# Kernel optimization log

Hardware: AMD Instinct MI355X
Metric: run time of the kernel (lower is better)

Reference implementation:

```python
import jax, jax.numpy as jnp
import numpy as np
import math

B, T, C = 64, 1024, 12
D, H, L = 512, 8, 2
FFN = 4 * D
FC_HIDDEN, NUM_CLASSES = 256, 5
KERNEL = 25          # config.moving_average default
FACTOR = 3           # config.autocorrelation_factor default
TOP_K = int(FACTOR * math.log(T))
EPS = 1e-5
MIN_SCALE = 1e-10


def _sinusoidal_pos(n_pos, dim):
    # HF AutoformerSinusoidalPositionalEmbedding._init_weight (Marian-style: sin block then cos block)
    pos = np.arange(n_pos, dtype=np.float64)[:, None]
    j = np.arange(dim)[None, :]
    enc = pos / np.power(10000.0, 2 * (j // 2) / dim)
    half = dim // 2
    out = np.zeros((n_pos, dim), np.float32)
    out[:, :half] = np.sin(enc[:, 0::2])
    out[:, half:] = np.cos(enc[:, 1::2])
    return jnp.asarray(out)


def _layernorm(x, g, b):
    mu = jnp.mean(x, axis=-1, keepdims=True)
    var = jnp.mean(jnp.square(x - mu), axis=-1, keepdims=True)
    return (x - mu) * jax.lax.rsqrt(var + EPS) * g + b


def _series_decomp_seasonal(x):
    # moving-average trend with edge-replication padding; return seasonal = x - trend
    pad = (KERNEL - 1) // 2
    xp = jnp.pad(x, ((0, 0), (pad, pad), (0, 0)), mode='edge')
    cs = jnp.cumsum(xp, axis=1)
    cs = jnp.concatenate([jnp.zeros_like(cs[:, :1]), cs], axis=1)
    trend = (cs[:, KERNEL:] - cs[:, :-KERNEL]) / KERNEL
    return x - trend


def _autocorr_attention(h, w, b):
    # w: (4, D, D) q/k/v/out, b: (4, D). Eval-mode HF AutoformerAttention (per-batch delays).
    hd = D // H
    def split(t):
        return t.reshape(B, T, H, hd).transpose(0, 2, 1, 3)  # (B,H,T,hd)
    q = split(h @ w[0] + b[0])
    k = split(h @ w[1] + b[1])
    v = split(h @ w[2] + b[2])
    # period-based dependency discovery via FFT cross-correlation along time
    qf = jnp.fft.rfft(q, n=T, axis=2)
    kf = jnp.fft.rfft(k, n=T, axis=2)
    corr = jnp.fft.irfft(qf * jnp.conj(kf), n=T, axis=2)  # (B,H,T,hd)
    mean_corr = corr.mean(axis=(1, 3))                    # (B,T)
    top_vals, top_idx = jax.lax.top_k(mean_corr, TOP_K)   # (B,K)
    wts = jax.nn.softmax(top_vals, axis=-1)               # (B,K)
    t_idx = jnp.arange(T)
    agg = jnp.zeros_like(v)
    for i in range(TOP_K):  # small fixed K, mirrors HF loop; circular roll by -delay
        idx = (t_idx[None, :] + top_idx[:, i][:, None]) % T      # (B,T)
        rolled = jnp.take_along_axis(v, idx[:, None, :, None], axis=2)
        agg = agg + rolled * wts[:, i][:, None, None, None]
    out = agg.transpose(0, 2, 1, 3).reshape(B, T, D)
    return out @ w[3] + b[3]


def _forward(x, emb_w, emb_ln_g, emb_ln_b, attn_w, attn_b, ln_g, ln_b,
             fc1_w, fc1_b, fc2_w, fc2_b, head_w1, head_b1, head_w2, head_b2):
    # AutoformerMeanScaler (observed mask is all-ones): scale = mean |x| over time, loc = 0
    scale = jnp.clip(jnp.mean(jnp.abs(x), axis=1, keepdims=True), MIN_SCALE)  # (B,1,C)
    inputs = x / scale
    # static features: log1p(|loc|)=0 and log(scale), broadcast over time; lags=[0] -> lagged == inputs
    static = jnp.concatenate([jnp.zeros_like(scale), jnp.log(scale)], axis=-1)  # (B,1,2C)
    feats = jnp.broadcast_to(static, (B, T, 2 * C))
    ti = jnp.concatenate([inputs, feats], axis=-1)  # (B,T,3C)

    h = ti @ emb_w + _sinusoidal_pos(T, D)[None]
    h = _layernorm(h, emb_ln_g, emb_ln_b)

    for l in range(L):
        res = h
        a = _autocorr_attention(h, attn_w[l], attn_b[l])
        h = _layernorm(res + a, ln_g[l, 0], ln_b[l, 0])
        h = _series_decomp_seasonal(h)
        res = h
        f = jax.nn.gelu(h @ fc1_w[l] + fc1_b[l], approximate=False)
        h = res + f @ fc2_w[l] + fc2_b[l]
        h = _layernorm(h, ln_g[l, 1], ln_b[l, 1])
        h = _series_decomp_seasonal(h)

    feat = h.mean(axis=1)  # (B,D)
    return jax.nn.relu(feat @ head_w1 + head_b1) @ head_w2 + head_b2  # (B,num_classes)


def setup_inputs() -> dict:
    key = jax.random.key(0)
    ks = jax.random.split(key, 8)
    s = 0.02
    rn = lambda k, shape: jax.random.normal(k, shape, jnp.float32) * s
    return {
        'x': jax.random.normal(ks[0], (B, T, C), jnp.float32),
        'emb_w': rn(ks[1], (3 * C, D)),
        'emb_ln_g': jnp.ones((D,), jnp.float32),
        'emb_ln_b': jnp.zeros((D,), jnp.float32),
        'attn_w': rn(ks[2], (L, 4, D, D)),
        'attn_b': jnp.zeros((L, 4, D), jnp.float32),
        'ln_g': jnp.ones((L, 2, D), jnp.float32),
        'ln_b': jnp.zeros((L, 2, D), jnp.float32),
        'fc1_w': rn(ks[3], (L, D, FFN)),
        'fc1_b': jnp.zeros((L, FFN), jnp.float32),
        'fc2_w': rn(ks[4], (L, FFN, D)),
        'fc2_b': jnp.zeros((L, D), jnp.float32),
        'head_w1': rn(ks[5], (D, FC_HIDDEN)),
        'head_b1': jnp.zeros((FC_HIDDEN,), jnp.float32),
        'head_w2': rn(ks[6], (FC_HIDDEN, NUM_CLASSES)),
        'head_b2': jnp.zeros((NUM_CLASSES,), jnp.float32),
    }


def reference(x, emb_w, emb_ln_g, emb_ln_b, attn_w, attn_b, ln_g, ln_b,
              fc1_w, fc1_b, fc2_w, fc2_b, head_w1, head_b1, head_w2, head_b2):
    return _forward(x, emb_w, emb_ln_g, emb_ln_b, attn_w, attn_b, ln_g, ln_b,
                    fc1_w, fc1_b, fc2_w, fc2_b, head_w1, head_b1, head_w2, head_b2)
```

## Files before the change

### kernel.cpp

```cpp
#include <hip/hip_runtime.h>
#include <math.h>

#define CB 64
#define CT 1024
#define CCH 12
#define CD 512
#define CL 2
#define CFFN 2048
#define CFCH 256
#define CNC 5
#define CTOPK 20
#define CEPS 1e-5f

typedef __attribute__((ext_vector_type(8))) short bfrag;
typedef __attribute__((ext_vector_type(4))) float ffrag;

__device__ inline ushort bf16r(float f) {
  unsigned u = __float_as_uint(f);
  unsigned r = (u + 0x7FFFu + ((u >> 16) & 1u)) >> 16;
  return (ushort)r;
}
__device__ inline float bf16f(ushort h) { return __uint_as_float(((unsigned)h) << 16); }

__device__ __forceinline__ void gld16(const ushort* g, ushort* l) {
  __builtin_amdgcn_global_load_lds((__attribute__((address_space(1))) void*)g,
                                   (__attribute__((address_space(3))) void*)l,
                                   16, 0, 0);
}

struct c32 { float x, y; };
__device__ inline c32 cadd(c32 a, c32 b) { return c32{a.x + b.x, a.y + b.y}; }
__device__ inline c32 csub(c32 a, c32 b) { return c32{a.x - b.x, a.y - b.y}; }
__device__ inline c32 cmul(c32 a, c32 b) {
  return c32{a.x * b.x - a.y * b.y, a.x * b.y + a.y * b.x};
}
__device__ inline c32 cmulj(c32 a, c32 b) {
  return c32{a.x * b.x + a.y * b.y, a.y * b.x - a.x * b.y};
}
__device__ inline c32 mineg_i(c32 a) { return c32{a.y, -a.x}; }
__device__ inline c32 mul_i(c32 a) { return c32{-a.y, a.x}; }

#define ZIDX(p) ((p) + ((p) >> 4))

__device__ inline int drev4(int t) {
  return ((t & 3) << 8) | (((t >> 2) & 3) << 6) | (((t >> 4) & 3) << 4) |
         (((t >> 6) & 3) << 2) | ((t >> 8) & 3);
}

template <int INV>
__device__ inline void fft_stage(c32* zz, const c32* twl, int tid, int s) {
  int L = 1 << (2 * s);
  int j = tid & (L - 1);
  int g = tid >> (2 * s);
  int p0 = (g << (2 * s + 2)) + j;
  int tb = j << (8 - 2 * s);
  c32 w1 = twl[ZIDX(tb)], w2 = twl[ZIDX(2 * tb)], w3 = twl[ZIDX(3 * tb)];
  c32 b0 = zz[ZIDX(p0)], b1 = zz[ZIDX(p0 + L)], b2 = zz[ZIDX(p0 + 2 * L)],
      b3 = zz[ZIDX(p0 + 3 * L)];
  if (INV) { b1 = cmulj(b1, w1); b2 = cmulj(b2, w2); b3 = cmulj(b3, w3); }
  else     { b1 = cmul(b1, w1);  b2 = cmul(b2, w2);  b3 = cmul(b3, w3); }
  c32 e0 = cadd(b0, b2), e1 = csub(b0, b2), e2 = cadd(b1, b3), e3 = csub(b1, b3);
  c32 e3r = INV ? mul_i(e3) : mineg_i(e3);
  zz[ZIDX(p0)] = cadd(e0, e2);
  zz[ZIDX(p0 + L)] = cadd(e1, e3r);
  zz[ZIDX(p0 + 2 * L)] = csub(e0, e2);
  zz[ZIDX(p0 + 3 * L)] = csub(e1, e3r);
}

__device__ inline void unp_acc(const c32* zf, int w, c32& acc) {
  int wc = (1024 - w) & 1023;
  c32 Z1 = zf[ZIDX(w)];
  c32 Z2r = zf[ZIDX(wc)];
  c32 Z2 = c32{Z2r.x, -Z2r.y};
  c32 Qf = c32{0.5f * (Z1.x + Z2.x), 0.5f * (Z1.y + Z2.y)};
  c32 M = c32{Z1.x - Z2.x, Z1.y - Z2.y};
  c32 Kf = c32{0.5f * M.y, -0.5f * M.x};
  acc.x += Qf.x * Kf.x + Qf.y * Kf.y;
  acc.y += Qf.y * Kf.x - Qf.x * Kf.y;
}

__global__ __launch_bounds__(256) void k_twid(c32* __restrict__ tw) {
  int j = blockIdx.x * 256 + threadIdx.x;
  double a = -2.0 * 3.14159265358979323846 * (double)j / 1024.0;
  tw[j] = c32{(float)cos(a), (float)sin(a)};
}

__global__ __launch_bounds__(256) void k_scale(const float* __restrict__ x,
                                               float* __restrict__ sc,
                                               float* __restrict__ lg) {
  int b = blockIdx.x, tid = threadIdx.x;
  float acc[CCH];
#pragma unroll
  for (int c = 0; c < CCH; ++c) acc[c] = 0.f;
  const float* xb = x + (size_t)b * CT * CCH;
  for (int t = tid; t < CT; t += 256) {
    const float* row = xb + t * CCH;
#pragma unroll
    for (int c = 0; c < CCH; ++c) acc[c] += fabsf(row[c]);
  }
  __shared__ float red[256][CCH];
#pragma unroll
  for (int c = 0; c < CCH; ++c) red[tid][c] = acc[c];
  __syncthreads();
  for (int off = 128; off > 0; off >>= 1) {
    if (tid < off) {
#pragma unroll
      for (int c = 0; c < CCH; ++c) red[tid][c] += red[tid + off][c];
    }
    __syncthreads();
  }
  if (tid < CCH) {
    float s = fmaxf(red[0][tid] * (1.0f / CT), 1e-10f);
    sc[b * CCH + tid] = s;
    lg[b * CCH + tid] = logf(s);
  }
}

__global__ __launch_bounds__(512) void k_postab(float* __restrict__ pos) {
  int t = blockIdx.x;
  int d = threadIdx.x;
  double v;
  if (d < 256) {
    double w = pow(10000.0, -((double)d) / 256.0);
    v = sin((double)t * w);
  } else {
    double w = pow(10000.0, -((double)(d - 256)) / 256.0);
    v = cos((double)t * w);
  }
  pos[(size_t)t * CD + d] = (float)v;
}

__global__ __launch_bounds__(128) void k_embed(const float* __restrict__ x,
                                               const float* __restrict__ sc,
                                               const float* __restrict__ lg,
                                               const float* __restrict__ W,
                                               const float* __restrict__ postab,
                                               const float* __restrict__ g,
                                               const float* __restrict__ beta,
                                               float* __restrict__ h,
                                               ushort* __restrict__ h2) {
  int row = blockIdx.x;
  int b = row >> 10, t = row & 1023;
  int tid = threadIdx.x;
  __shared__ float xs[CCH], ls[CCH];
  if (tid < CCH) {
    float s = sc[b * CCH + tid];
    xs[tid] = x[(size_t)row * CCH + tid] / s;
    ls[tid] = lg[b * CCH + tid];
  }
  __syncthreads();
  int d0 = tid * 4;
  float4 p = *(const float4*)(postab + (size_t)t * CD + d0);
  float v0 = p.x, v1 = p.y, v2 = p.z, v3 = p.w;
#pragma unroll
  for (int c = 0; c < CCH; ++c) {
    float xc = xs[c], lc = ls[c];
    float4 w0 = *(const float4*)(W + (size_t)c * CD + d0);
    float4 w1 = *(const float4*)(W + (size_t)(24 + c) * CD + d0);
    v0 += xc * w0.x + lc * w1.x;
    v1 += xc * w0.y + lc * w1.y;
    v2 += xc * w0.z + lc * w1.z;
    v3 += xc * w0.w + lc * w1.w;
  }
  float s1 = v0 + v1 + v2 + v3;
  float s2 = v0 * v0 + v1 * v1 + v2 * v2 + v3 * v3;
  for (int off = 32; off > 0; off >>= 1) {
    s1 += __shfl_down(s1, off);
    s2 += __shfl_down(s2, off);
  }
  __shared__ float ws1[2], ws2[2], mv[2];
  int wid = tid >> 6, lane = tid & 63;
  if (lane == 0) { ws1[wid] = s1; ws2[wid] = s2; }
  __syncthreads();
  if (tid == 0) {
    float S1 = ws1[0] + ws1[1], S2 = ws2[0] + ws2[1];
    float mu = S1 * (1.0f / CD);
    float var = S2 * (1.0f / CD) - mu * mu;
    mv[0] = mu;
    mv[1] = 1.0f / sqrtf(var + CEPS);
  }
  __syncthreads();
  float mu = mv[0], ri = mv[1];
  float4 gg = *(const float4*)(g + d0);
  float4 bb = *(const float4*)(beta + d0);
  float4 o;
  o.x = (v0 - mu) * ri * gg.x + bb.x;
  o.y = (v1 - mu) * ri * gg.y + bb.y;
  o.z = (v2 - mu) * ri * gg.z + bb.z;
  o.w = (v3 - mu) * ri * gg.w + bb.w;
  *(float4*)(h + (size_t)row * CD + d0) = o;
  ushort4 hv = {bf16r(o.x), bf16r(o.y), bf16r(o.z), bf16r(o.w)};
  *(ushort4*)(h2 + (size_t)row * CD + d0) = hv;
}

__global__ __launch_bounds__(256) void k_cvtw(const float* __restrict__ W,
                                              ushort* __restrict__ W2,
                                              int K, int N) {
  __shared__ float tile[32][33];
  int tx = threadIdx.x & 31, ty = threadIdx.x >> 5;
  int n0 = blockIdx.x * 32, k0 = blockIdx.y * 32;
#pragma unroll
  for (int r = 0; r < 4; ++r)
    tile[ty * 4 + r][tx] = W[(size_t)(k0 + ty * 4 + r) * N + n0 + tx];
  __syncthreads();
#pragma unroll
  for (int r = 0; r < 4; ++r) {
    int nl = ty * 4 + r, kl = tx;
    W2[(size_t)(n0 + nl) * K + k0 + kl] = bf16r(tile[kl][nl]);
  }
}

template <int EPI>
__global__ __launch_bounds__(256) void k_gemm3(const ushort* __restrict__ A,
                                               const ushort* __restrict__ W,
                                               const float* __restrict__ bias,
                                               const float* __restrict__ R,
                                               float* __restrict__ Cf,
                                               ushort* __restrict__ Cs,
                                               ushort* __restrict__ Cs2,
                                               int lda, int ldb, int ldc, int K) {
  __shared__ ushort AhS[2][128 * 32];
  __shared__ ushort BhS[2][128 * 32];
  int tid = threadIdx.x;
  int n0 = blockIdx.x * 128, m0 = blockIdx.y * 128;
  int wid = __builtin_amdgcn_readfirstlane(tid >> 6);
  int lane = tid & 63;
  int lr = lane >> 2;
  int lc = ((lane & 3) ^ ((lr >> 2) & 3)) * 8;
  int wm = wid >> 1, wn = wid & 1;
  int mOff = wm * 64, nOff = wn * 64;
  int quad = lane >> 4, l16 = lane & 15;

  const ushort* pA = A + (size_t)(m0 + wid * 32 + lr) * lda + lc;
  const ushort* pB = W + (size_t)(n0 + wid * 32 + lr) * ldb + lc;
  const int NK = K >> 5;

  ffrag acc[4][4];
#pragma unroll
  for (int i = 0; i < 4; ++i)
#pragma unroll
    for (int j = 0; j < 4; ++j) acc[i][j] = (ffrag)(0.f);

#define ISSUE(t, buf)                                                        \
  {                                                                          \
    int kk = (t) << 5;                                                       \
    ushort* lA = &AhS[buf][(wid * 32) * 32];                                 \
    ushort* lB = &BhS[buf][(wid * 32) * 32];                                 \
    gld16(pA + kk, lA);                                                      \
    gld16(pA + (size_t)16 * lda + kk, lA + 16 * 32);                         \
    gld16(pB + kk, lB);                                                      \
    gld16(pB + (size_t)16 * ldb + kk, lB + 16 * 32);                         \
  }

  ISSUE(0, 0);
  ISSUE(1, 1);
  for (int k = 0; k < NK; ++k) {
    if (k + 1 < NK) {
      asm volatile("s_waitcnt vmcnt(4)\n\ts_barrier" ::: "memory");
    } else {
      asm volatile("s_waitcnt vmcnt(0)\n\ts_barrier" ::: "memory");
    }
    int buf = k & 1;
    bfrag ah[4], bh[4];
#pragma unroll
    for (int i = 0; i < 4; ++i) {
      int row = mOff + i * 16 + l16;
      ah[i] = *(const bfrag*)&AhS[buf][row * 32 + (quad ^ ((row >> 2) & 3)) * 8];
    }
#pragma unroll
    for (int j = 0; j < 4; ++j) {
      int row = nOff + j * 16 + l16;
      bh[j] = *(const bfrag*)&BhS[buf][row * 32 + (quad ^ ((row >> 2) & 3)) * 8];
    }
#pragma unroll
    for (int i = 0; i < 4; ++i)
#pragma unroll
      for (int j = 0; j < 4; ++j)
        acc[i][j] = __builtin_amdgcn_mfma_f32_16x16x32_bf16(ah[i], bh[j], acc[i][j], 0, 0, 0);
    asm volatile("s_barrier" ::: "memory");
    if (k + 2 < NK) ISSUE(k + 2, buf);
  }
#undef ISSUE

#pragma unroll
  for (int j = 0; j < 4; ++j) {
    int col = n0 + nOff + j * 16 + l16;
    float bcol = bias[col];
#pragma unroll
    for (int i = 0; i < 4; ++i) {
      int rowb = m0 + mOff + i * 16 + quad * 4;
      if (EPI == 7) {
        if (col < 1024) {
          float4 o = {acc[i][j][0] + bcol, acc[i][j][1] + bcol,
                      acc[i][j][2] + bcol, acc[i][j][3] + bcol};
          *(float4*)(Cf + (size_t)col * ldc + rowb) = o;
        } else {
          float* Vf = (float*)Cs;
#pragma unroll
          for (int r = 0; r < 4; ++r)
            Vf[(size_t)(rowb + r) * 512 + (col - 1024)] = acc[i][j][r] + bcol;
        }
      } else {
#pragma unroll
        for (int r = 0; r < 4; ++r) {
          int row = rowb + r;
          float vv = acc[i][j][r] + bcol;
          if (EPI == 1) vv = 0.5f * vv * (1.0f + erff(vv * 0.7071067811865475f));
          if (EPI == 2) vv += R[(size_t)row * ldc + col];
          if (EPI == 1) {
            Cs[(size_t)row * ldc + col] = bf16r(vv);
          } else {
            Cf[(size_t)row * ldc + col] = vv;
          }
        }
      }
    }
  }
}

__global__ __launch_bounds__(256) void k_fft(const float* __restrict__ QT,
                                             const c32* __restrict__ twg,
                                             c32* __restrict__ part, int Mc) {
  __shared__ c32 z[4][1088];
  __shared__ c32 twl[1088];
  int dg = blockIdx.x, zb = blockIdx.y, tid = threadIdx.x;
#pragma unroll
  for (int k = 0; k < 4; ++k) {
    int i = tid + k * 256;
    twl[ZIDX(i)] = twg[i];
  }
  c32 pa = {0.f, 0.f}, pb = {0.f, 0.f}, p5 = {0.f, 0.f};
  for (int i = 0; i < 4; ++i) {
    int d0 = dg * 16 + i * 4;
#pragma unroll
    for (int f = 0; f < 4; ++f) {
      const float* qr = QT + (size_t)(d0 + f) * Mc + (size_t)zb * 1024;
      const float* kr = QT + (size_t)(512 + d0 + f) * Mc + (size_t)zb * 1024;
#pragma unroll
      for (int k = 0; k < 4; ++k) {
        int t = tid + k * 256;
        z[f][ZIDX(drev4(t))] = c32{qr[t], kr[t]};
      }
    }
    __syncthreads();
    for (int s = 0; s < 5; ++s) {
#pragma unroll
      for (int f = 0; f < 4; ++f) fft_stage<0>(&z[f][0], twl, tid, s);
      __syncthreads();
    }
#pragma unroll
    for (int f = 0; f < 4; ++f) {
      unp_acc(&z[f][0], tid, pa);
      unp_acc(&z[f][0], tid + 256, pb);
      if (tid == 0) unp_acc(&z[f][0], 512, p5);
    }
    __syncthreads();
  }
  c32* po = part + ((size_t)zb * 32 + dg) * 513;
  po[tid] = pa;
  po[tid + 256] = pb;
  if (tid == 0) po[512] = p5;
}

__global__ __launch_bounds__(256) void k_spectopk(const c32* __restrict__ part,
                                                  const c32* __restrict__ twg,
                                                  float* __restrict__ wts,
                                                  int* __restrict__ idxs) {
  int b = blockIdx.x, tid = threadIdx.x;
  __shared__ c32 twl[1088];
  __shared__ c32 S[1024];
  __shared__ c32 zz[1088];
  __shared__ float corr[1024];
#pragma unroll
  for (int k = 0; k < 4; ++k) {
    int i = tid + k * 256;
    twl[ZIDX(i)] = twg[i];
  }
  c32 sa = {0.f, 0.f}, sb = {0.f, 0.f}, s5 = {0.f, 0.f};
  const c32* pbase = part + (size_t)b * 32 * 513;
  for (int p = 0; p < 32; ++p) {
    const c32* pp = pbase + p * 513;
    sa = cadd(sa, pp[tid]);
    sb = cadd(sb, pp[tid + 256]);
    if (tid == 0) s5 = cadd(s5, pp[512]);
  }
  S[tid] = sa;
  S[tid + 256] = sb;
  if (tid == 0) S[512] = s5;
  if (tid > 0) S[1024 - tid] = c32{sa.x, -sa.y};
  S[768 - tid] = c32{sb.x, -sb.y};
  __syncthreads();
#pragma unroll
  for (int k = 0; k < 4; ++k) {
    int t = tid + k * 256;
    zz[ZIDX(drev4(t))] = S[t];
  }
  __syncthreads();
  for (int s = 0; s < 5; ++s) {
    fft_stage<1>(&zz[0], twl, tid, s);
    __syncthreads();
  }
  const float scl = 1.0f / (1024.0f * 512.0f);
#pragma unroll
  for (int k = 0; k < 4; ++k) {
    int t = tid + k * 256;
    corr[t] = zz[ZIDX(t)].x * scl;
  }
  __syncthreads();
  __shared__ float swv[4];
  __shared__ int swi[4];
  __shared__ float selv[CTOPK];
  __shared__ int seli[CTOPK];
  int wid = tid >> 6, lane = tid & 63;
  for (int k = 0; k < CTOPK; ++k) {
    float bv = -INFINITY;
    int bi = 0;
#pragma unroll
    for (int q = 0; q < 4; ++q) {
      int idx = tid + q * 256;
      float v = corr[idx];
      if (v > bv || (v == bv && idx < bi)) { bv = v; bi = idx; }
    }
#pragma unroll
    for (int off = 32; off > 0; off >>= 1) {
      float ov = __shfl_down(bv, off);
      int oi = __shfl_down(bi, off);
      if (ov > bv || (ov == bv && oi < bi)) { bv = ov; bi = oi; }
    }
    if (lane == 0) { swv[wid] = bv; swi[wid] = bi; }
    __syncthreads();
    if (tid == 0) {
      float mvv = swv[0];
      int mi = swi[0];
      for (int q2 = 1; q2 < 4; ++q2)
        if (swv[q2] > mvv || (swv[q2] == mvv && swi[q2] < mi)) { mvv = swv[q2]; mi = swi[q2]; }
      selv[k] = mvv;
      seli[k] = mi;
      corr[mi] = -INFINITY;
    }
    __syncthreads();
  }
  if (tid == 0) {
    float mx = selv[0], sum = 0.f, e[CTOPK];
    for (int k = 0; k < CTOPK; ++k) {
      e[k] = expf(selv[k] - mx);
      sum += e[k];
    }
    float inv = 1.0f / sum;
    for (int k = 0; k < CTOPK; ++k) {
      wts[b * CTOPK + k] = e[k] * inv;
      idxs[b * CTOPK + k] = seli[k];
    }
  }
}

__global__ __launch_bounds__(128) void k_agg(const float* __restrict__ Vf,
                                             const float* __restrict__ wts,
                                             const int* __restrict__ idxs,
                                             ushort* __restrict__ out2) {
  int nb = gridDim.x;
  int blk = blockIdx.x;
  int row = (blk & 7) * (nb >> 3) + (blk >> 3);
  int b = row >> 10, t = row & 1023;
  int d0 = threadIdx.x * 4;
  const float* Vb = Vf + (size_t)b * CT * 512;
  float4 acc = {0.f, 0.f, 0.f, 0.f};
#pragma unroll
  for (int k = 0; k < CTOPK; ++k) {
    float w = wts[b * CTOPK + k];
    int r = t + idxs[b * CTOPK + k];
    if (r >= CT) r -= CT;
    float4 v = *(const float4*)(Vb + (size_t)r * 512 + d0);
    acc.x += w * v.x;
    acc.y += w * v.y;
    acc.z += w * v.z;
    acc.w += w * v.w;
  }
  ushort4 hv = {bf16r(acc.x), bf16r(acc.y), bf16r(acc.z), bf16r(acc.w)};
  *(ushort4*)(out2 + (size_t)row * CD + d0) = hv;
}

template <int ADD>
__global__ __launch_bounds__(128) void k_ln(const float* __restrict__ X,
                                            const float* __restrict__ Rr,
                                            const float* __restrict__ g,
                                            const float* __restrict__ beta,
                                            float* __restrict__ out) {
  int row = blockIdx.x, tid = threadIdx.x;
  int d0 = tid * 4;
  float4 v = *(const float4*)(X + (size_t)row * CD + d0);
  if (ADD) {
    float4 r = *(const float4*)(Rr + (size_t)row * CD + d0);
    v.x += r.x; v.y += r.y; v.z += r.z; v.w += r.w;
  }
  float s1 = v.x + v.y + v.z + v.w;
  float s2 = v.x * v.x + v.y * v.y + v.z * v.z + v.w * v.w;
  for (int off = 32; off > 0; off >>= 1) {
    s1 += __shfl_down(s1, off);
    s2 += __shfl_down(s2, off);
  }
  __shared__ float ws1[2], ws2[2], mv[2];
  int wid = tid >> 6, lane = tid & 63;
  if (lane == 0) { ws1[wid] = s1; ws2[wid] = s2; }
  __syncthreads();
  if (tid == 0) {
    float S1 = ws1[0] + ws1[1], S2 = ws2[0] + ws2[1];
    float mu = S1 * (1.0f / CD);
    float var = S2 * (1.0f / CD) - mu * mu;
    mv[0] = mu;
    mv[1] = 1.0f / sqrtf(var + CEPS);
  }
  __syncthreads();
  float mu = mv[0], ri = mv[1];
  float4 gg = *(const float4*)(g + d0);
  float4 bb = *(const float4*)(beta + d0);
  float4 o;
  o.x = (v.x - mu) * ri * gg.x + bb.x;
  o.y = (v.y - mu) * ri * gg.y + bb.y;
  o.z = (v.z - mu) * ri * gg.z + bb.z;
  o.w = (v.w - mu) * ri * gg.w + bb.w;
  *(float4*)(out + (size_t)row * CD + d0) = o;
}

__global__ __launch_bounds__(128) void k_decomp(const float* __restrict__ X,
                                                float* __restrict__ out,
                                                ushort* __restrict__ out2) {
  int nb = gridDim.x;
  int blk = blockIdx.x;
  int row = (blk & 7) * (nb >> 3) + (blk >> 3);
  int b = row >> 10, t = row & 1023;
  int d0 = threadIdx.x * 4;
  const float* xb = X + (size_t)b * CT * CD + d0;
  float4 s = {0.f, 0.f, 0.f, 0.f};
#pragma unroll
  for (int j = -12; j <= 12; ++j) {
    int tt = t + j;
    tt = tt < 0 ? 0 : (tt > CT - 1 ? CT - 1 : tt);
    float4 v = *(const float4*)(xb + (size_t)tt * CD);
    s.x += v.x; s.y += v.y; s.z += v.z; s.w += v.w;
  }
  float4 xv = *(const float4*)(xb + (size_t)t * CD);
  const float inv = 1.0f / 25.0f;
  float4 o = {xv.x - s.x * inv, xv.y - s.y * inv, xv.z - s.z * inv, xv.w - s.w * inv};
  *(float4*)(out + (size_t)row * CD + d0) = o;
  ushort4 hv = {bf16r(o.x), bf16r(o.y), bf16r(o.z), bf16r(o.w)};
  *(ushort4*)(out2 + (size_t)row * CD + d0) = hv;
}

__global__ __launch_bounds__(256) void k_meanp(const float* __restrict__ X,
                                               float* __restrict__ part) {
  int b = blockIdx.x, g = blockIdx.y, tid = threadIdx.x;
  const float* xb = X + (size_t)b * CT * CD + (size_t)g * 128 * CD;
  float a0 = 0.f, a1 = 0.f;
  for (int r = 0; r < 128; ++r) {
    a0 += xb[(size_t)r * CD + tid];
    a1 += xb[(size_t)r * CD + tid + 256];
  }
  part[((size_t)b * 8 + g) * CD + tid] = a0;
  part[((size_t)b * 8 + g) * CD + tid + 256] = a1;
}

__global__ __launch_bounds__(256) void k_headf(const float* __restrict__ part,
                                               const float* __restrict__ w1,
                                               const float* __restrict__ b1,
                                               const float* __restrict__ w2,
                                               const float* __restrict__ b2,
                                               float* __restrict__ out) {
  int b = blockIdx.x, tid = threadIdx.x;
  __shared__ float f[CD];
  __shared__ float hid[CFCH];
  for (int d = tid; d < CD; d += 256) {
    float s = 0.f;
#pragma unroll
    for (int g = 0; g < 8; ++g) s += part[((size_t)b * 8 + g) * CD + d];
    f[d] = s * (1.0f / CT);
  }
  __syncthreads();
  float a = b1[tid];
  for (int d = 0; d < CD; ++d) a += f[d] * w1[d * CFCH + tid];
  hid[tid] = fmaxf(a, 0.f);
  __syncthreads();
  if (tid < CNC) {
    float a2 = b2[tid];
    for (int j = 0; j < CFCH; ++j) a2 += hid[j] * w2[j * CNC + tid];
    out[b * CNC + tid] = a2;
  }
}

extern "C" void kernel_launch(void* const* d_in, const int* in_sizes, int n_in,
                              void* d_out, int out_size, void* d_ws, size_t ws_size,
                              hipStream_t stream) {
  const float* x = (const float*)d_in[0];
  const float* emb_w = (const float*)d_in[1];
  const float* emb_g = (const float*)d_in[2];
  const float* emb_b = (const float*)d_in[3];
  const float* attn_w = (const float*)d_in[4];
  const float* attn_b = (const float*)d_in[5];
  const float* ln_g = (const float*)d_in[6];
  const float* ln_bb = (const float*)d_in[7];
  const float* fc1_w = (const float*)d_in[8];
  const float* fc1_b = (const float*)d_in[9];
  const float* fc2_w = (const float*)d_in[10];
  const float* fc2_b = (const float*)d_in[11];
  const float* hw1 = (const float*)d_in[12];
  const float* hb1 = (const float*)d_in[13];
  const float* hw2 = (const float*)d_in[14];
  const float* hb2 = (const float*)d_in[15];
  float* outp = (float*)d_out;

  const size_t WQ = 262144ULL;
  const size_t LW = 4 * WQ + 1048576ULL + 1048576ULL;
  const size_t W2TOT = CL * LW;

  const size_t FIXED_B = W2TOT * 2
                         + (size_t)CT * CD * 4
                         + 2 * (size_t)CB * CCH * 4
                         + 2 * (size_t)CB * CTOPK * 4
                         + (size_t)CB * 8 * CD * 4
                         + 1024 * 8
                         + 4096;
  const size_t PERB = 2ULL * CT * CD * 4 + (size_t)CT * CD * 2 + (size_t)CT * 2048 * 2 +
                      (size_t)32 * 513 * 8;
  int Bc = CB;
  while (Bc > 1) {
    if ((size_t)Bc * PERB + FIXED_B <= ws_size) break;
    Bc >>= 1;
  }
  const size_t CHF = (size_t)Bc * CT * CD;

  char* wsp = (char*)d_ws;
  float* P0 = (float*)wsp;     wsp += CHF * 4;
  float* P1 = (float*)wsp;     wsp += CHF * 4;
  ushort* U0 = (ushort*)wsp;   wsp += CHF * 2;
  ushort* U1 = (ushort*)wsp;   wsp += (size_t)Bc * CT * 2048 * 2;
  ushort* W2b = (ushort*)wsp;  wsp += W2TOT * 2;
  float* postab = (float*)wsp; wsp += (size_t)CT * CD * 4;
  float* scb = (float*)wsp;    wsp += (size_t)CB * CCH * 4;
  float* lgb = (float*)wsp;    wsp += (size_t)CB * CCH * 4;
  float* wtb = (float*)wsp;    wsp += (size_t)CB * CTOPK * 4;
  int* idb = (int*)wsp;        wsp += (size_t)CB * CTOPK * 4;
  float* partb = (float*)wsp;  wsp += (size_t)CB * 8 * CD * 4;
  c32* twc = (c32*)wsp;        wsp += 1024 * sizeof(c32);
  c32* partc = (c32*)wsp;      wsp += (size_t)Bc * 32 * 513 * sizeof(c32);

  for (int l = 0; l < CL; ++l) {
    ushort* wq2 = W2b + l * LW;
    ushort* wo2 = wq2 + 3 * WQ;
    ushort* w12 = wo2 + WQ;
    ushort* w22 = w12 + 1048576;
    for (int m = 0; m < 4; ++m)
      k_cvtw<<<dim3(CD / 32, CD / 32), 256, 0, stream>>>(
          attn_w + ((size_t)(l * 4 + m)) * CD * CD, wq2 + m * WQ, CD, CD);
    k_cvtw<<<dim3(CFFN / 32, CD / 32), 256, 0, stream>>>(
        fc1_w + (size_t)l * CD * CFFN, w12, CD, CFFN);
    k_cvtw<<<dim3(CD / 32, CFFN / 32), 256, 0, stream>>>(
        fc2_w + (size_t)l * CFFN * CD, w22, CFFN, CD);
  }

  k_scale<<<CB, 256, 0, stream>>>(x, scb, lgb);
  k_postab<<<CT, 512, 0, stream>>>(postab);
  k_twid<<<4, 256, 0, stream>>>(twc);

  for (int b0 = 0; b0 < CB; b0 += Bc) {
    const int Mc = Bc * CT;

    float* HP = P0;
    float* SA = P1;

    k_embed<<<Mc, 128, 0, stream>>>(x + (size_t)b0 * CT * CCH, scb + b0 * CCH,
                                    lgb + b0 * CCH, emb_w, postab, emb_g, emb_b,
                                    HP, U0);

    for (int l = 0; l < CL; ++l) {
      const float* bqkv = attn_b + (size_t)l * 4 * CD;
      const float* bo = attn_b + (size_t)(l * 4 + 3) * CD;
      const float* g0 = ln_g + (size_t)(l * 2 + 0) * CD;
      const float* be0 = ln_bb + (size_t)(l * 2 + 0) * CD;
      const float* g1 = ln_g + (size_t)(l * 2 + 1) * CD;
      const float* be1 = ln_bb + (size_t)(l * 2 + 1) * CD;
      const float* B1 = fc1_b + (size_t)l * CFFN;
      const float* B2f = fc2_b + (size_t)l * CD;
      const ushort* wq2 = W2b + l * LW;
      const ushort* wo2 = wq2 + 3 * WQ;
      const ushort* w12 = wo2 + WQ;
      const ushort* w22 = w12 + 1048576;

      k_gemm3<7><<<dim3(1536 / 128, Mc / 128), 256, 0, stream>>>(
          U0, wq2, bqkv, nullptr, (float*)U1, (ushort*)SA, nullptr, CD, CD, Mc, CD);
      k_fft<<<dim3(32, Bc), 256, 0, stream>>>((const float*)U1, twc, partc, Mc);
      k_spectopk<<<Bc, 256, 0, stream>>>(partc, twc, wtb, idb);
      k_agg<<<Mc, 128, 0, stream>>>((const float*)SA, wtb, idb, U0);
      k_gemm3<2><<<dim3(CD / 128, Mc / 128), 256, 0, stream>>>(
          U0, wo2, bo, HP, SA, nullptr, nullptr, CD, CD, CD, CD);
      k_ln<0><<<Mc, 128, 0, stream>>>(SA, nullptr, g0, be0, HP);
      k_decomp<<<Mc, 128, 0, stream>>>(HP, SA, U0);
      k_gemm3<1><<<dim3(CFFN / 128, Mc / 128), 256, 0, stream>>>(
          U0, w12, B1, nullptr, nullptr, U1, nullptr, CD, CD, CFFN, CD);
      k_gemm3<2><<<dim3(CD / 128, Mc / 128), 256, 0, stream>>>(
          U1, w22, B2f, SA, HP, nullptr, nullptr, CFFN, CFFN, CD, CFFN);
      k_ln<0><<<Mc, 128, 0, stream>>>(HP, nullptr, g1, be1, HP);
      k_decomp<<<Mc, 128, 0, stream>>>(HP, SA, U0);
      float* t = HP;
      HP = SA;
      SA = t;
    }

    k_meanp<<<dim3(Bc, 8), 256, 0, stream>>>(HP, partb + (size_t)b0 * 8 * CD);
    k_headf<<<Bc, 256, 0, stream>>>(partb + (size_t)b0 * 8 * CD, hw1, hb1, hw2, hb2,
                                    outp + (size_t)b0 * CNC);
  }
}
```

Baseline: 3.305 ms.

## Triple-buffer GEMM loads, swizzle workgroups, fuse layernorm into decomposition

```diff
diff --git a/kernel.cpp b/kernel.cpp
--- a/kernel.cpp
+++ b/kernel.cpp
@@ -219,10 +219,14 @@
                                                ushort* __restrict__ Cs,
                                                ushort* __restrict__ Cs2,
                                                int lda, int ldb, int ldc, int K) {
-  __shared__ ushort AhS[2][128 * 32];
-  __shared__ ushort BhS[2][128 * 32];
+  __shared__ ushort AhS[3][128 * 32];
+  __shared__ ushort BhS[3][128 * 32];
   int tid = threadIdx.x;
-  int n0 = blockIdx.x * 128, m0 = blockIdx.y * 128;
+  int nx = gridDim.x;
+  int nwg = nx * gridDim.y;
+  int flat = blockIdx.y * nx + blockIdx.x;
+  int sw = (flat & 7) * (nwg >> 3) + (flat >> 3);
+  int n0 = (sw % nx) * 128, m0 = (sw / nx) * 128;
   int wid = __builtin_amdgcn_readfirstlane(tid >> 6);
   int lane = tid & 63;
   int lr = lane >> 2;
@@ -254,13 +258,16 @@
 
   ISSUE(0, 0);
   ISSUE(1, 1);
+  ISSUE(2, 2);
   for (int k = 0; k < NK; ++k) {
-    if (k + 1 < NK) {
+    if (k + 2 < NK) {
+      asm volatile("s_waitcnt vmcnt(8)\n\ts_barrier" ::: "memory");
+    } else if (k + 1 < NK) {
       asm volatile("s_waitcnt vmcnt(4)\n\ts_barrier" ::: "memory");
     } else {
       asm volatile("s_waitcnt vmcnt(0)\n\ts_barrier" ::: "memory");
     }
-    int buf = k & 1;
+    int buf = k % 3;
     bfrag ah[4], bh[4];
 #pragma unroll
     for (int i = 0; i < 4; ++i) {
@@ -278,7 +285,7 @@
       for (int j = 0; j < 4; ++j)
         acc[i][j] = __builtin_amdgcn_mfma_f32_16x16x32_bf16(ah[i], bh[j], acc[i][j], 0, 0, 0);
     asm volatile("s_barrier" ::: "memory");
-    if (k + 2 < NK) ISSUE(k + 2, buf);
+    if (k + 3 < NK) ISSUE(k + 3, (k + 3) % 3);
   }
 #undef ISSUE
 
@@ -480,26 +487,18 @@
   *(ushort4*)(out2 + (size_t)row * CD + d0) = hv;
 }
 
-template <int ADD>
-__global__ __launch_bounds__(128) void k_ln(const float* __restrict__ X,
-                                            const float* __restrict__ Rr,
-                                            const float* __restrict__ g,
-                                            const float* __restrict__ beta,
-                                            float* __restrict__ out) {
+__global__ __launch_bounds__(128) void k_stats(const float* __restrict__ X,
+                                               c32* __restrict__ st) {
   int row = blockIdx.x, tid = threadIdx.x;
   int d0 = tid * 4;
   float4 v = *(const float4*)(X + (size_t)row * CD + d0);
-  if (ADD) {
-    float4 r = *(const float4*)(Rr + (size_t)row * CD + d0);
-    v.x += r.x; v.y += r.y; v.z += r.z; v.w += r.w;
-  }
   float s1 = v.x + v.y + v.z + v.w;
   float s2 = v.x * v.x + v.y * v.y + v.z * v.z + v.w * v.w;
   for (int off = 32; off > 0; off >>= 1) {
     s1 += __shfl_down(s1, off);
     s2 += __shfl_down(s2, off);
   }
-  __shared__ float ws1[2], ws2[2], mv[2];
+  __shared__ float ws1[2], ws2[2];
   int wid = tid >> 6, lane = tid & 63;
   if (lane == 0) { ws1[wid] = s1; ws2[wid] = s2; }
   __syncthreads();
@@ -507,41 +506,43 @@
     float S1 = ws1[0] + ws1[1], S2 = ws2[0] + ws2[1];
     float mu = S1 * (1.0f / CD);
     float var = S2 * (1.0f / CD) - mu * mu;
-    mv[0] = mu;
-    mv[1] = 1.0f / sqrtf(var + CEPS);
-  }
-  __syncthreads();
-  float mu = mv[0], ri = mv[1];
-  float4 gg = *(const float4*)(g + d0);
-  float4 bb = *(const float4*)(beta + d0);
-  float4 o;
-  o.x = (v.x - mu) * ri * gg.x + bb.x;
-  o.y = (v.y - mu) * ri * gg.y + bb.y;
-  o.z = (v.z - mu) * ri * gg.z + bb.z;
-  o.w = (v.w - mu) * ri * gg.w + bb.w;
-  *(float4*)(out + (size_t)row * CD + d0) = o;
-}
-
-__global__ __launch_bounds__(128) void k_decomp(const float* __restrict__ X,
-                                                float* __restrict__ out,
-                                                ushort* __restrict__ out2) {
+    st[row] = c32{mu, 1.0f / sqrtf(var + CEPS)};
+  }
+}
+
+__global__ __launch_bounds__(128) void k_dec2(const float* __restrict__ X,
+                                              const c32* __restrict__ st,
+                                              const float* __restrict__ g,
+                                              float* __restrict__ out,
+                                              ushort* __restrict__ out2) {
   int nb = gridDim.x;
   int blk = blockIdx.x;
   int row = (blk & 7) * (nb >> 3) + (blk >> 3);
   int b = row >> 10, t = row & 1023;
   int d0 = threadIdx.x * 4;
   const float* xb = X + (size_t)b * CT * CD + d0;
+  const c32* sb = st + (size_t)b * CT;
   float4 s = {0.f, 0.f, 0.f, 0.f};
 #pragma unroll
   for (int j = -12; j <= 12; ++j) {
     int tt = t + j;
     tt = tt < 0 ? 0 : (tt > CT - 1 ? CT - 1 : tt);
+    c32 ms = sb[tt];
     float4 v = *(const float4*)(xb + (size_t)tt * CD);
-    s.x += v.x; s.y += v.y; s.z += v.z; s.w += v.w;
-  }
+    s.x += (v.x - ms.x) * ms.y;
+    s.y += (v.y - ms.x) * ms.y;
+    s.z += (v.z - ms.x) * ms.y;
+    s.w += (v.w - ms.x) * ms.y;
+  }
+  c32 mc = sb[t];
   float4 xv = *(const float4*)(xb + (size_t)t * CD);
+  float4 gg = *(const float4*)(g + d0);
   const float inv = 1.0f / 25.0f;
-  float4 o = {xv.x - s.x * inv, xv.y - s.y * inv, xv.z - s.z * inv, xv.w - s.w * inv};
+  float4 o;
+  o.x = gg.x * ((xv.x - mc.x) * mc.y - s.x * inv);
+  o.y = gg.y * ((xv.y - mc.x) * mc.y - s.y * inv);
+  o.z = gg.z * ((xv.z - mc.x) * mc.y - s.z * inv);
+  o.w = gg.w * ((xv.w - mc.x) * mc.y - s.w * inv);
   *(float4*)(out + (size_t)row * CD + d0) = o;
   ushort4 hv = {bf16r(o.x), bf16r(o.y), bf16r(o.z), bf16r(o.w)};
   *(ushort4*)(out2 + (size_t)row * CD + d0) = hv;
@@ -620,7 +621,7 @@
                          + 1024 * 8
                          + 4096;
   const size_t PERB = 2ULL * CT * CD * 4 + (size_t)CT * CD * 2 + (size_t)CT * 2048 * 2 +
-                      (size_t)32 * 513 * 8;
+                      (size_t)32 * 513 * 8 + (size_t)CT * 8;
   int Bc = CB;
   while (Bc > 1) {
     if ((size_t)Bc * PERB + FIXED_B <= ws_size) break;
@@ -642,6 +643,7 @@
   float* partb = (float*)wsp;  wsp += (size_t)CB * 8 * CD * 4;
   c32* twc = (c32*)wsp;        wsp += 1024 * sizeof(c32);
   c32* partc = (c32*)wsp;      wsp += (size_t)Bc * 32 * 513 * sizeof(c32);
+  c32* stb = (c32*)wsp;        wsp += (size_t)Bc * CT * sizeof(c32);
 
   for (int l = 0; l < CL; ++l) {
     ushort* wq2 = W2b + l * LW;
@@ -675,9 +677,7 @@
       const float* bqkv = attn_b + (size_t)l * 4 * CD;
       const float* bo = attn_b + (size_t)(l * 4 + 3) * CD;
       const float* g0 = ln_g + (size_t)(l * 2 + 0) * CD;
-      const float* be0 = ln_bb + (size_t)(l * 2 + 0) * CD;
       const float* g1 = ln_g + (size_t)(l * 2 + 1) * CD;
-      const float* be1 = ln_bb + (size_t)(l * 2 + 1) * CD;
       const float* B1 = fc1_b + (size_t)l * CFFN;
       const float* B2f = fc2_b + (size_t)l * CD;
       const ushort* wq2 = W2b + l * LW;
@@ -692,17 +692,14 @@
       k_agg<<<Mc, 128, 0, stream>>>((const float*)SA, wtb, idb, U0);
       k_gemm3<2><<<dim3(CD / 128, Mc / 128), 256, 0, stream>>>(
           U0, wo2, bo, HP, SA, nullptr, nullptr, CD, CD, CD, CD);
-      k_ln<0><<<Mc, 128, 0, stream>>>(SA, nullptr, g0, be0, HP);
-      k_decomp<<<Mc, 128, 0, stream>>>(HP, SA, U0);
+      k_stats<<<Mc, 128, 0, stream>>>(SA, stb);
+      k_dec2<<<Mc, 128, 0, stream>>>(SA, stb, g0, HP, U0);
       k_gemm3<1><<<dim3(CFFN / 128, Mc / 128), 256, 0, stream>>>(
           U0, w12, B1, nullptr, nullptr, U1, nullptr, CD, CD, CFFN, CD);
       k_gemm3<2><<<dim3(CD / 128, Mc / 128), 256, 0, stream>>>(
-          U1, w22, B2f, SA, HP, nullptr, nullptr, CFFN, CFFN, CD, CFFN);
-      k_ln<0><<<Mc, 128, 0, stream>>>(HP, nullptr, g1, be1, HP);
-      k_decomp<<<Mc, 128, 0, stream>>>(HP, SA, U0);
-      float* t = HP;
-      HP = SA;
-      SA = t;
+          U1, w22, B2f, HP, SA, nullptr, nullptr, CFFN, CFFN, CD, CFFN);
+      k_stats<<<Mc, 128, 0, stream>>>(SA, stb);
+      k_dec2<<<Mc, 128, 0, stream>>>(SA, stb, g1, HP, U0);
     }
 
     k_meanp<<<dim3(Bc, 8), 256, 0, stream>>>(HP, partb + (size_t)b0 * 8 * CD);
```

After: 3.125 ms. -5.4%, faster.
